# Kernel tuning notes

Hardware: AMD Instinct MI355X
Metric: run time of the kernel (lower is better)

## Reference

```python
import jax, jax.numpy as jnp
import numpy as np

H, N, CH, L = 256, 256, 1, 1024


def setup_inputs() -> dict:
    key = jax.random.key(0)
    k1, k2, k3, k4 = jax.random.split(key, 4)
    # Hurwitz-like A so the discretized dA is stable (|eig| < 1) over L powers
    A = 0.05 * jax.random.normal(k1, (H, N, N), jnp.float32) - jnp.eye(N, dtype=jnp.float32)
    B = jax.random.normal(k2, (H, N), jnp.float32)
    C = jax.random.normal(k3, (CH, H, N), jnp.float32)
    log_dt = jax.random.uniform(k4, (H,), jnp.float32,
                                minval=np.log(1e-3), maxval=np.log(1e-1))
    return {"A": A, "B": B, "C": C, "log_dt": log_dt}


def reference(A, B, C, log_dt):
    # Bilinear (Tustin) discretization:
    #   dA = (I - dt/2 A)^{-1} (I + dt/2 A),  dB = dt * (I - dt/2 A)^{-1} B
    dt = jnp.exp(log_dt)                                   # (H,)
    I = jnp.eye(A.shape[-1], dtype=A.dtype)
    A_bwd = I - (dt[:, None, None] / 2) * A                # (H, N, N)
    A_fwd = I + (dt[:, None, None] / 2) * A                # (H, N, N)
    dB = dt[:, None] * jnp.linalg.solve(A_bwd, B[..., None])[..., 0]   # (H, N)
    dA = jnp.linalg.solve(A_bwd, A_fwd)                    # (H, N, N)

    # Krylov kernel: k[c,h,l] = C[c,h,:] @ dA^l @ dB[h,:]
    def step(x, _):
        y = jnp.einsum('chn,hn->ch', C, x)                 # contract with C
        x_next = jnp.einsum('hmn,hn->hm', dA, x)           # advance state
        return x_next, y

    _, ys = jax.lax.scan(step, dB, None, length=L)         # ys: (L, CH, H)
    k = jnp.transpose(ys, (1, 2, 0))                       # (CH, H, L)
    return k
```

## Files before the change

kernel.cpp:

```cpp
#include <hip/hip_runtime.h>
#include <cstdint>
#include <cstddef>

#define NH 256
#define ND 256
#define NL 1024
#define NUV 16
#define NWV 64

typedef __attribute__((ext_vector_type(4))) float f32x4;
typedef __attribute__((ext_vector_type(8))) short short8;
typedef __attribute__((ext_vector_type(8))) unsigned short u16x8;
typedef __attribute__((ext_vector_type(4))) unsigned short u16x4;
typedef __attribute__((ext_vector_type(4))) unsigned int u32x4;

__device__ __forceinline__ float bfrec(unsigned short hi, unsigned short lo) {
  return __uint_as_float(((unsigned)hi) << 16) + __uint_as_float(((unsigned)lo) << 16);
}
__device__ __forceinline__ unsigned rne16(unsigned u) {
  return u + 0x7FFFu + ((u >> 16) & 1u);
}
__device__ __forceinline__ void bfsplit(float x, unsigned short& hi, unsigned short& lo) {
  unsigned u = __float_as_uint(x);
  unsigned r1 = rne16(u);
  hi = (unsigned short)(r1 >> 16);
  float lf = x - __uint_as_float(r1 & 0xFFFF0000u);
  unsigned r2 = rne16(__float_as_uint(lf));
  lo = (unsigned short)(r2 >> 16);
}
__device__ __forceinline__ void gload16(const void* g, void* l) {
  __builtin_amdgcn_global_load_lds(
      (const __attribute__((address_space(1))) unsigned int*)g,
      (__attribute__((address_space(3))) unsigned int*)l, 16, 0, 0);
}
__device__ __forceinline__ int ksw(int row) { return (row >> 1) & 3; }

__global__ __launch_bounds__(256) void prep_kernel(
    const float* __restrict__ A, const float* __restrict__ log_dt,
    unsigned short* __restrict__ Mhi, unsigned short* __restrict__ Mlo)
{
  size_t e0 = ((size_t)blockIdx.x * 256 + threadIdx.x) * 16;
  int h = (int)(e0 >> 16);
  float hdt = 0.5f * __expf(log_dt[h]);
  unsigned short hb[16], lb[16];
#pragma unroll
  for (int i = 0; i < 4; ++i) {
    f32x4 v = *(const f32x4*)(A + e0 + i * 4);
#pragma unroll
    for (int j = 0; j < 4; ++j) bfsplit(v[j] * hdt, hb[i * 4 + j], lb[i * 4 + j]);
  }
  unsigned ph[8], pl[8];
#pragma unroll
  for (int i = 0; i < 8; ++i) {
    ph[i] = (unsigned)hb[2 * i] | ((unsigned)hb[2 * i + 1] << 16);
    pl[i] = (unsigned)lb[2 * i] | ((unsigned)lb[2 * i + 1] << 16);
  }
  u32x4 a0 = {ph[0], ph[1], ph[2], ph[3]}, a1 = {ph[4], ph[5], ph[6], ph[7]};
  u32x4 b0 = {pl[0], pl[1], pl[2], pl[3]}, b1 = {pl[4], pl[5], pl[6], pl[7]};
  *(u32x4*)(Mhi + e0) = a0; *(u32x4*)(Mhi + e0 + 8) = a1;
  *(u32x4*)(Mlo + e0) = b0; *(u32x4*)(Mlo + e0 + 8) = b1;
}

template <int ADDX, int QOUT>
__global__ __launch_bounds__(256) void gemm128_kernel(
    const unsigned short* __restrict__ Xhi, const unsigned short* __restrict__ Xlo,
    const unsigned short* __restrict__ Yhi, const unsigned short* __restrict__ Ylo,
    unsigned short* __restrict__ Dhi, unsigned short* __restrict__ Dlo,
    unsigned short* __restrict__ Qhi, unsigned short* __restrict__ Qlo)
{
  __shared__ unsigned short lds[33792];
  int tid = threadIdx.x;
  int lane = tid & 63, w = tid >> 6;
  int bid = blockIdx.x;
  int h = bid & 255, part = bid >> 8;
  int m0 = (part >> 1) * 128, n0 = (part & 1) * 128;
  size_t mb = (size_t)h * 65536;

  f32x4 acc[2][8];
#pragma unroll
  for (int m = 0; m < 2; ++m)
#pragma unroll
    for (int n = 0; n < 8; ++n) { f32x4 z = {0.f, 0.f, 0.f, 0.f}; acc[m][n] = z; }

  auto STAGE = [&](int s, int kb) {
#pragma unroll
    for (int j = 0; j < 2; ++j) {
      int c = j * 256 + tid;
      {
        int row = c >> 2, sp = c & 3;
        size_t go = mb + (size_t)(m0 + row) * 256 + kb * 32 + ((sp ^ ksw(row)) << 3);
        gload16(Xhi + go, &lds[s * 8192 + c * 8]);
        gload16(Xlo + go, &lds[s * 8192 + 4096 + c * 8]);
      }
      {
        int k = c >> 4, ns = c & 15;
        size_t go = mb + (size_t)(kb * 32 + k) * 256 + n0 + ns * 8;
        gload16(Yhi + go, &lds[16384 + s * 8192 + c * 8]);
        gload16(Ylo + go, &lds[16384 + s * 8192 + 4096 + c * 8]);
      }
    }
  };

  STAGE(0, 0);
  __builtin_amdgcn_sched_barrier(0);

  int nn = tid & 127, kh = tid >> 7;
  int cur = 0;
  for (int kb = 0; kb < 8; ++kb) {
    int nxt = cur ^ 1;
    if (kb < 7) {
      STAGE(nxt, kb + 1);
      __builtin_amdgcn_sched_barrier(0);
      asm volatile("s_waitcnt vmcnt(8)" ::: "memory");
    } else {
      asm volatile("s_waitcnt vmcnt(0)" ::: "memory");
    }
    __builtin_amdgcn_sched_barrier(0);
    __builtin_amdgcn_s_barrier();
    __builtin_amdgcn_sched_barrier(0);

    unsigned short* yb = &lds[16384 + cur * 8192];
    unsigned short rh[16], rl[16];
#pragma unroll
    for (int i = 0; i < 16; ++i) {
      rh[i] = yb[(kh * 16 + i) * 128 + nn];
      rl[i] = yb[4096 + (kh * 16 + i) * 128 + nn];
    }
    asm volatile("s_waitcnt lgkmcnt(0)" ::: "memory");
    __builtin_amdgcn_sched_barrier(0);
    __builtin_amdgcn_s_barrier();
    __builtin_amdgcn_sched_barrier(0);

#pragma unroll
    for (int s2 = 0; s2 < 2; ++s2) {
      int sl = kh * 2 + s2;
      int off = nn * 32 + ((sl ^ ksw(nn)) << 3);
      u16x8 vh, vl;
#pragma unroll
      for (int e = 0; e < 8; ++e) { vh[e] = rh[s2 * 8 + e]; vl[e] = rl[s2 * 8 + e]; }
      *(u16x8*)&yb[off] = vh;
      *(u16x8*)&yb[4096 + off] = vl;
    }
    asm volatile("s_waitcnt lgkmcnt(0)" ::: "memory");
    __builtin_amdgcn_sched_barrier(0);
    __builtin_amdgcn_s_barrier();
    __builtin_amdgcn_sched_barrier(0);

    int kg = lane >> 4, li = lane & 15;
    const unsigned short* xb = &lds[cur * 8192];
    short8 bhi[8], blo[8];
#pragma unroll
    for (int n = 0; n < 8; ++n) {
      int rowN = n * 16 + li;
      int off = rowN * 32 + ((kg ^ ksw(rowN)) << 3);
      bhi[n] = *(const short8*)&yb[off];
      blo[n] = *(const short8*)&yb[4096 + off];
    }
    __builtin_amdgcn_s_setprio(1);
#pragma unroll
    for (int m = 0; m < 2; ++m) {
      int rowM = w * 32 + m * 16 + li;
      int off = rowM * 32 + ((kg ^ ksw(rowM)) << 3);
      short8 ahi = *(const short8*)&xb[off];
      short8 alo = *(const short8*)&xb[4096 + off];
#pragma unroll
      for (int n = 0; n < 8; ++n) {
        acc[m][n] = __builtin_amdgcn_mfma_f32_16x16x32_bf16(ahi, bhi[n], acc[m][n], 0, 0, 0);
        acc[m][n] = __builtin_amdgcn_mfma_f32_16x16x32_bf16(ahi, blo[n], acc[m][n], 0, 0, 0);
        acc[m][n] = __builtin_amdgcn_mfma_f32_16x16x32_bf16(alo, bhi[n], acc[m][n], 0, 0, 0);
      }
    }
    __builtin_amdgcn_s_setprio(0);
    __builtin_amdgcn_sched_barrier(0);
    __builtin_amdgcn_s_barrier();
    __builtin_amdgcn_sched_barrier(0);
    cur = nxt;
  }

  float* fb = (float*)lds;
  {
    int q0 = (lane >> 4) * 4, li = lane & 15;
#pragma unroll
    for (int m = 0; m < 2; ++m)
#pragma unroll
      for (int n = 0; n < 8; ++n)
#pragma unroll
        for (int q = 0; q < 4; ++q)
          fb[(w * 32 + m * 16 + q0 + q) * 132 + n * 16 + li] = acc[m][n][q];
  }
  __syncthreads();
  {
    int row = tid >> 1, half = tid & 1;
#pragma unroll 1
    for (int hp = 0; hp < 2; ++hp) {
      int c0 = half * 64 + hp * 32;
      float v[32];
#pragma unroll
      for (int u = 0; u < 8; ++u) {
        f32x4 t4 = *(const f32x4*)&fb[row * 132 + c0 + u * 4];
#pragma unroll
        for (int e = 0; e < 4; ++e) v[u * 4 + e] = t4[e];
      }
      size_t go = mb + (size_t)(m0 + row) * 256 + n0 + c0;
      float xv[32];
      if (ADDX || QOUT) {
#pragma unroll
        for (int u = 0; u < 4; ++u) {
          u16x8 xh = *(const u16x8*)(Xhi + go + u * 8);
          u16x8 xl = *(const u16x8*)(Xlo + go + u * 8);
#pragma unroll
          for (int e = 0; e < 8; ++e) xv[u * 8 + e] = bfrec(xh[e], xl[e]);
        }
        if (ADDX) {
#pragma unroll
          for (int e = 0; e < 32; ++e) v[e] += xv[e];
        }
      }
      {
        unsigned hw[16], lw[16];
#pragma unroll
        for (int i = 0; i < 16; ++i) {
          unsigned short ha, la, hb2, lb2;
          bfsplit(v[2 * i], ha, la);
          bfsplit(v[2 * i + 1], hb2, lb2);
          hw[i] = (unsigned)ha | ((unsigned)hb2 << 16);
          lw[i] = (unsigned)la | ((unsigned)lb2 << 16);
        }
#pragma unroll
        for (int u = 0; u < 4; ++u) {
          u32x4 a = {hw[u * 4], hw[u * 4 + 1], hw[u * 4 + 2], hw[u * 4 + 3]};
          u32x4 b = {lw[u * 4], lw[u * 4 + 1], lw[u * 4 + 2], lw[u * 4 + 3]};
          *(u32x4*)(Dhi + go + u * 8) = a;
          *(u32x4*)(Dlo + go + u * 8) = b;
        }
      }
      if (QOUT) {
        int grow = m0 + row, gc0 = n0 + c0;
        float qv[32];
#pragma unroll
        for (int e = 0; e < 32; ++e)
          qv[e] = v[e] + 2.f * xv[e] + ((gc0 + e) == grow ? 1.f : 0.f);
        unsigned hw[16], lw[16];
#pragma unroll
        for (int i = 0; i < 16; ++i) {
          unsigned short ha, la, hb2, lb2;
          bfsplit(qv[2 * i], ha, la);
          bfsplit(qv[2 * i + 1], hb2, lb2);
          hw[i] = (unsigned)ha | ((unsigned)hb2 << 16);
          lw[i] = (unsigned)la | ((unsigned)lb2 << 16);
        }
#pragma unroll
        for (int u = 0; u < 4; ++u) {
          u32x4 a = {hw[u * 4], hw[u * 4 + 1], hw[u * 4 + 2], hw[u * 4 + 3]};
          u32x4 b = {lw[u * 4], lw[u * 4 + 1], lw[u * 4 + 2], lw[u * 4 + 3]};
          *(u32x4*)(Qhi + go + u * 8) = a;
          *(u32x4*)(Qlo + go + u * 8) = b;
        }
      }
    }
  }
}

__global__ __launch_bounds__(256) void db_kernel(
    const unsigned short* __restrict__ dAhi, const unsigned short* __restrict__ dAlo,
    const float* __restrict__ Bv, const float* __restrict__ log_dt, float* __restrict__ dB)
{
  int h = blockIdx.x, r = threadIdx.x;
  __shared__ float bl[256];
  bl[r] = Bv[h * 256 + r];
  __syncthreads();
  const unsigned short* ph = dAhi + (size_t)h * 65536 + (size_t)r * 256;
  const unsigned short* pl = dAlo + (size_t)h * 65536 + (size_t)r * 256;
  float acc = bl[r];
  for (int c8 = 0; c8 < 32; ++c8) {
    u16x8 vh = *(const u16x8*)(ph + c8 * 8);
    u16x8 vl = *(const u16x8*)(pl + c8 * 8);
#pragma unroll
    for (int e = 0; e < 8; ++e) acc += bfrec(vh[e], vl[e]) * bl[c8 * 8 + e];
  }
  dB[h * 256 + r] = 0.5f * __expf(log_dt[h]) * acc;
}

__device__ __forceinline__ int physc(int c) { return c + ((c >> 4) << 2); }

__global__ __launch_bounds__(1024) void chain_kernel(
    const unsigned short* __restrict__ dAhi, const unsigned short* __restrict__ dAlo,
    const unsigned short* __restrict__ Ghi, const unsigned short* __restrict__ Glo,
    const float* __restrict__ Cin, const float* __restrict__ dB,
    float* __restrict__ U, float* __restrict__ W)
{
  int b = blockIdx.x;
  bool um = b < NH;
  int h = um ? b : b - NH;
  const float* x0 = um ? (Cin + (size_t)h * 256) : (dB + (size_t)h * 256);
  float* out = um ? (U + (size_t)h * (NUV * 256)) : (W + (size_t)h * (NWV * 256));
  int nv = um ? NUV : NWV;

  int tid = threadIdx.x;
  int rg = tid >> 4, cg = tid & 15;
  float mat[4][16];
  if (um) {
    const unsigned short* mh = dAhi + (size_t)h * 65536;
    const unsigned short* ml = dAlo + (size_t)h * 65536;
#pragma unroll
    for (int j = 0; j < 16; ++j) {
      u16x4 h4 = *(const u16x4*)(mh + (size_t)(cg * 16 + j) * 256 + rg * 4);
      u16x4 l4 = *(const u16x4*)(ml + (size_t)(cg * 16 + j) * 256 + rg * 4);
#pragma unroll
      for (int rr = 0; rr < 4; ++rr) mat[rr][j] = bfrec(h4[rr], l4[rr]);
    }
  } else {
    const unsigned short* mh = Ghi + (size_t)h * 65536;
    const unsigned short* ml = Glo + (size_t)h * 65536;
#pragma unroll
    for (int rr = 0; rr < 4; ++rr) {
      const unsigned short* ph = mh + (size_t)(rg * 4 + rr) * 256 + cg * 16;
      const unsigned short* pl = ml + (size_t)(rg * 4 + rr) * 256 + cg * 16;
      u16x8 h0 = *(const u16x8*)ph, h1 = *(const u16x8*)(ph + 8);
      u16x8 l0 = *(const u16x8*)pl, l1 = *(const u16x8*)(pl + 8);
#pragma unroll
      for (int e = 0; e < 8; ++e) {
        mat[rr][e] = bfrec(h0[e], l0[e]);
        mat[rr][8 + e] = bfrec(h1[e], l1[e]);
      }
    }
  }
  __shared__ float xb[2][320];
  if (tid < 256) {
    float vv = x0[tid];
    xb[0][physc(tid)] = vv;
    out[tid] = vv;
  }
  __syncthreads();
  int p = 0;
  for (int v = 1; v < nv; ++v) {
    float part[4] = {0.f, 0.f, 0.f, 0.f};
#pragma unroll
    for (int sl = 0; sl < 4; ++sl) {
      f32x4 xv = *(const f32x4*)&xb[p][cg * 20 + sl * 4];
#pragma unroll
      for (int rr = 0; rr < 4; ++rr)
#pragma unroll
        for (int e = 0; e < 4; ++e) part[rr] += mat[rr][sl * 4 + e] * xv[e];
    }
#pragma unroll
    for (int rr = 0; rr < 4; ++rr) {
      part[rr] += __shfl_xor(part[rr], 1, 64);
      part[rr] += __shfl_xor(part[rr], 2, 64);
      part[rr] += __shfl_xor(part[rr], 4, 64);
      part[rr] += __shfl_xor(part[rr], 8, 64);
    }
    float val = (cg == 0) ? part[0] : ((cg == 1) ? part[1] : ((cg == 2) ? part[2] : part[3]));
    if (cg < 4) {
      int row = rg * 4 + cg;
      xb[p ^ 1][physc(row)] = val;
      out[(size_t)v * 256 + row] = val;
    }
    __syncthreads();
    p ^= 1;
  }
}

__global__ __launch_bounds__(512) void gram_kernel(
    const float* __restrict__ U, const float* __restrict__ W, float* __restrict__ out)
{
  int b = blockIdx.x;
  int h = b >> 1, jh = b & 1;
  __shared__ float ul[16][260];
  __shared__ float wl[32][260];
  int tid = threadIdx.x;
  const float* Up = U + (size_t)h * (NUV * 256);
  const float* Wp = W + (size_t)h * (NWV * 256) + (size_t)jh * 32 * 256;
  {
    int r = tid >> 5, cb = (tid & 31) * 8;
    f32x4 a = *(const f32x4*)(Up + (size_t)r * 256 + cb);
    f32x4 c2 = *(const f32x4*)(Up + (size_t)r * 256 + cb + 4);
    *(f32x4*)&ul[r][cb] = a;
    *(f32x4*)&ul[r][cb + 4] = c2;
  }
  {
    int r = tid >> 4, cb = (tid & 15) * 16;
#pragma unroll
    for (int u = 0; u < 4; ++u) {
      f32x4 a = *(const f32x4*)(Wp + (size_t)r * 256 + cb + u * 4);
      *(f32x4*)&wl[r][cb + u * 4] = a;
    }
  }
  __syncthreads();
  int i = tid >> 5, j2 = tid & 31;
  float acc = 0.f;
#pragma unroll 8
  for (int c = 0; c < 256; c += 4) {
    f32x4 uu = *(const f32x4*)&ul[i][c];
    f32x4 ww = *(const f32x4*)&wl[j2][c];
    acc += uu[0] * ww[0] + uu[1] * ww[1] + uu[2] * ww[2] + uu[3] * ww[3];
  }
  out[(size_t)h * 1024 + (size_t)(jh * 32 + j2) * 16 + i] = acc;
}

__global__ void bail_kernel(float* out, unsigned mib) {
  if (threadIdx.x == 0) out[blockIdx.x] = -(2.0e6f + (float)mib * 4096.0f);
}

extern "C" void kernel_launch(void* const* d_in, const int* in_sizes, int n_in,
                              void* d_out, int out_size, void* d_ws, size_t ws_size,
                              hipStream_t stream) {
  const float* A = (const float*)d_in[0];
  const float* B = (const float*)d_in[1];
  const float* C = (const float*)d_in[2];
  const float* log_dt = (const float*)d_in[3];
  float* out = (float*)d_out;

  const size_t BUF = (size_t)NH * ND * ND * 2 * 2;
  const size_t HALF = (size_t)NH * ND * ND;
  const size_t VEC = (size_t)NH * ND * 4;
  const size_t USZ = (size_t)NH * NUV * ND * 4;
  const size_t WSZ = (size_t)NH * NWV * ND * 4;
  const size_t NEED3 = 3 * BUF + VEC + USZ + WSZ;
  if (ws_size < NEED3) {
    bail_kernel<<<8, 64, 0, stream>>>(out, (unsigned)(ws_size >> 20));
    return;
  }
  uint8_t* w8 = (uint8_t*)d_ws;
  auto HI = [&](int b) -> unsigned short* { return (unsigned short*)(w8 + (size_t)b * BUF); };
  auto LO = [&](int b) -> unsigned short* { return HI(b) + HALF; };
  float* dBp = (float*)(w8 + 3 * BUF);
  float* Up = (float*)(w8 + 3 * BUF + VEC);
  float* Wp = (float*)(w8 + 3 * BUF + VEC + USZ);

  prep_kernel<<<4096, 256, 0, stream>>>(A, log_dt, HI(0), LO(0));
  gemm128_kernel<0, 1><<<1024, 256, 0, stream>>>(HI(0), LO(0), HI(0), LO(0),
                                                 HI(1), LO(1), HI(2), LO(2));
  gemm128_kernel<1, 0><<<1024, 256, 0, stream>>>(HI(2), LO(2), HI(1), LO(1),
                                                 HI(0), LO(0), nullptr, nullptr);
  gemm128_kernel<0, 0><<<1024, 256, 0, stream>>>(HI(1), LO(1), HI(1), LO(1),
                                                 HI(2), LO(2), nullptr, nullptr);
  gemm128_kernel<1, 0><<<1024, 256, 0, stream>>>(HI(0), LO(0), HI(2), LO(2),
                                                 HI(1), LO(1), nullptr, nullptr);
  db_kernel<<<NH, 256, 0, stream>>>(HI(1), LO(1), B, log_dt, dBp);
  gemm128_kernel<0, 0><<<1024, 256, 0, stream>>>(HI(1), LO(1), HI(1), LO(1),
                                                 HI(0), LO(0), nullptr, nullptr);
  gemm128_kernel<0, 0><<<1024, 256, 0, stream>>>(HI(0), LO(0), HI(0), LO(0),
                                                 HI(2), LO(2), nullptr, nullptr);
  gemm128_kernel<0, 0><<<1024, 256, 0, stream>>>(HI(2), LO(2), HI(2), LO(2),
                                                 HI(0), LO(0), nullptr, nullptr);
  gemm128_kernel<0, 0><<<1024, 256, 0, stream>>>(HI(0), LO(0), HI(0), LO(0),
                                                 HI(2), LO(2), nullptr, nullptr);
  chain_kernel<<<2 * NH, 1024, 0, stream>>>(HI(1), LO(1), HI(2), LO(2), C, dBp, Up, Wp);
  gram_kernel<<<2 * NH, 512, 0, stream>>>(Up, Wp, out);
}
```

Before: 650.3 us.

## Emit transposed GEMM outputs so consumers load B operand K-contiguous, skipping LDS transpose

The GEMM kernel gains template flags to also write a transposed copy of its result. Later GEMMs can then read the Y operand already in K-contiguous layout and drop the in-LDS transpose step with its extra barriers. The chain kernel is split so the U/W power chains read pre-transposed or row-major matrices directly. Workspace tiers pick how many planes are available, falling back to the old schedule when memory is short. The extra transposed stores add write traffic and memory footprint in exchange for cheaper GEMM inner loops.

```diff
diff --git a/kernel.cpp b/kernel.cpp
--- a/kernel.cpp
+++ b/kernel.cpp
@@ -61,11 +61,12 @@
   *(u32x4*)(Mlo + e0) = b0; *(u32x4*)(Mlo + e0 + 8) = b1;
 }
 
-template <int ADDX, int QOUT>
+template <int YT, int ADDX, int OUTN, int OUTT, int QOUT>
 __global__ __launch_bounds__(256) void gemm128_kernel(
     const unsigned short* __restrict__ Xhi, const unsigned short* __restrict__ Xlo,
     const unsigned short* __restrict__ Yhi, const unsigned short* __restrict__ Ylo,
     unsigned short* __restrict__ Dhi, unsigned short* __restrict__ Dlo,
+    unsigned short* __restrict__ DThi, unsigned short* __restrict__ DTlo,
     unsigned short* __restrict__ Qhi, unsigned short* __restrict__ Qlo)
 {
   __shared__ unsigned short lds[33792];
@@ -86,17 +87,28 @@
 #pragma unroll
     for (int j = 0; j < 2; ++j) {
       int c = j * 256 + tid;
-      {
+      if (YT) {
         int row = c >> 2, sp = c & 3;
-        size_t go = mb + (size_t)(m0 + row) * 256 + kb * 32 + ((sp ^ ksw(row)) << 3);
-        gload16(Xhi + go, &lds[s * 8192 + c * 8]);
-        gload16(Xlo + go, &lds[s * 8192 + 4096 + c * 8]);
-      }
-      {
-        int k = c >> 4, ns = c & 15;
-        size_t go = mb + (size_t)(kb * 32 + k) * 256 + n0 + ns * 8;
-        gload16(Yhi + go, &lds[16384 + s * 8192 + c * 8]);
-        gload16(Ylo + go, &lds[16384 + s * 8192 + 4096 + c * 8]);
+        int koff = kb * 32 + ((sp ^ ksw(row)) << 3);
+        size_t gx = mb + (size_t)(m0 + row) * 256 + koff;
+        size_t gy = mb + (size_t)(n0 + row) * 256 + koff;
+        gload16(Xhi + gx, &lds[s * 8192 + c * 8]);
+        gload16(Xlo + gx, &lds[s * 8192 + 4096 + c * 8]);
+        gload16(Yhi + gy, &lds[16384 + s * 8192 + c * 8]);
+        gload16(Ylo + gy, &lds[16384 + s * 8192 + 4096 + c * 8]);
+      } else {
+        {
+          int row = c >> 2, sp = c & 3;
+          size_t go = mb + (size_t)(m0 + row) * 256 + kb * 32 + ((sp ^ ksw(row)) << 3);
+          gload16(Xhi + go, &lds[s * 8192 + c * 8]);
+          gload16(Xlo + go, &lds[s * 8192 + 4096 + c * 8]);
+        }
+        {
+          int k = c >> 4, ns = c & 15;
+          size_t go = mb + (size_t)(kb * 32 + k) * 256 + n0 + ns * 8;
+          gload16(Yhi + go, &lds[16384 + s * 8192 + c * 8]);
+          gload16(Ylo + go, &lds[16384 + s * 8192 + 4096 + c * 8]);
+        }
       }
     }
   };
@@ -120,31 +132,32 @@
     __builtin_amdgcn_sched_barrier(0);
 
     unsigned short* yb = &lds[16384 + cur * 8192];
-    unsigned short rh[16], rl[16];
-#pragma unroll
-    for (int i = 0; i < 16; ++i) {
-      rh[i] = yb[(kh * 16 + i) * 128 + nn];
-      rl[i] = yb[4096 + (kh * 16 + i) * 128 + nn];
-    }
-    asm volatile("s_waitcnt lgkmcnt(0)" ::: "memory");
-    __builtin_amdgcn_sched_barrier(0);
-    __builtin_amdgcn_s_barrier();
-    __builtin_amdgcn_sched_barrier(0);
-
-#pragma unroll
-    for (int s2 = 0; s2 < 2; ++s2) {
-      int sl = kh * 2 + s2;
-      int off = nn * 32 + ((sl ^ ksw(nn)) << 3);
-      u16x8 vh, vl;
-#pragma unroll
-      for (int e = 0; e < 8; ++e) { vh[e] = rh[s2 * 8 + e]; vl[e] = rl[s2 * 8 + e]; }
-      *(u16x8*)&yb[off] = vh;
-      *(u16x8*)&yb[4096 + off] = vl;
-    }
-    asm volatile("s_waitcnt lgkmcnt(0)" ::: "memory");
-    __builtin_amdgcn_sched_barrier(0);
-    __builtin_amdgcn_s_barrier();
-    __builtin_amdgcn_sched_barrier(0);
+    if (!YT) {
+      unsigned short rh[16], rl[16];
+#pragma unroll
+      for (int i = 0; i < 16; ++i) {
+        rh[i] = yb[(kh * 16 + i) * 128 + nn];
+        rl[i] = yb[4096 + (kh * 16 + i) * 128 + nn];
+      }
+      asm volatile("s_waitcnt lgkmcnt(0)" ::: "memory");
+      __builtin_amdgcn_sched_barrier(0);
+      __builtin_amdgcn_s_barrier();
+      __builtin_amdgcn_sched_barrier(0);
+#pragma unroll
+      for (int s2 = 0; s2 < 2; ++s2) {
+        int sl = kh * 2 + s2;
+        int off = nn * 32 + ((sl ^ ksw(nn)) << 3);
+        u16x8 vh, vl;
+#pragma unroll
+        for (int e = 0; e < 8; ++e) { vh[e] = rh[s2 * 8 + e]; vl[e] = rl[s2 * 8 + e]; }
+        *(u16x8*)&yb[off] = vh;
+        *(u16x8*)&yb[4096 + off] = vl;
+      }
+      asm volatile("s_waitcnt lgkmcnt(0)" ::: "memory");
+      __builtin_amdgcn_sched_barrier(0);
+      __builtin_amdgcn_s_barrier();
+      __builtin_amdgcn_sched_barrier(0);
+    }
 
     int kg = lane >> 4, li = lane & 15;
     const unsigned short* xb = &lds[cur * 8192];
@@ -189,7 +202,7 @@
           fb[(w * 32 + m * 16 + q0 + q) * 132 + n * 16 + li] = acc[m][n][q];
   }
   __syncthreads();
-  {
+  if (OUTN || ADDX) {
     int row = tid >> 1, half = tid & 1;
 #pragma unroll 1
     for (int hp = 0; hp < 2; ++hp) {
@@ -214,9 +227,18 @@
         if (ADDX) {
 #pragma unroll
           for (int e = 0; e < 32; ++e) v[e] += xv[e];
-        }
-      }
-      {
+          if (OUTT) {
+#pragma unroll
+            for (int u = 0; u < 8; ++u) {
+              f32x4 t4;
+#pragma unroll
+              for (int e = 0; e < 4; ++e) t4[e] = v[u * 4 + e];
+              *(f32x4*)&fb[row * 132 + c0 + u * 4] = t4;
+            }
+          }
+        }
+      }
+      if (OUTN) {
         unsigned hw[16], lw[16];
 #pragma unroll
         for (int i = 0; i < 16; ++i) {
@@ -256,6 +278,34 @@
           *(u32x4*)(Qhi + go + u * 8) = a;
           *(u32x4*)(Qlo + go + u * 8) = b;
         }
+      }
+    }
+  }
+  if (OUTT) {
+    if (ADDX) __syncthreads();
+    int c = tid & 127, rh2 = tid >> 7;
+#pragma unroll 1
+    for (int ch2 = 0; ch2 < 2; ++ch2) {
+      int r0 = rh2 * 64 + ch2 * 32;
+      float tv[32];
+#pragma unroll
+      for (int i = 0; i < 32; ++i) tv[i] = fb[(r0 + i) * 132 + c];
+      unsigned hw[16], lw[16];
+#pragma unroll
+      for (int i = 0; i < 16; ++i) {
+        unsigned short ha, la, hb2, lb2;
+        bfsplit(tv[2 * i], ha, la);
+        bfsplit(tv[2 * i + 1], hb2, lb2);
+        hw[i] = (unsigned)ha | ((unsigned)hb2 << 16);
+        lw[i] = (unsigned)la | ((unsigned)lb2 << 16);
+      }
+      size_t go = mb + (size_t)(n0 + c) * 256 + m0 + r0;
+#pragma unroll
+      for (int u = 0; u < 4; ++u) {
+        u32x4 a = {hw[u * 4], hw[u * 4 + 1], hw[u * 4 + 2], hw[u * 4 + 3]};
+        u32x4 b = {lw[u * 4], lw[u * 4 + 1], lw[u * 4 + 2], lw[u * 4 + 3]};
+        *(u32x4*)(DThi + go + u * 8) = a;
+        *(u32x4*)(DTlo + go + u * 8) = b;
       }
     }
   }
@@ -283,7 +333,73 @@
 
 __device__ __forceinline__ int physc(int c) { return c + ((c >> 4) << 2); }
 
-__global__ __launch_bounds__(1024) void chain_kernel(
+__global__ __launch_bounds__(1024) void chainAB_kernel(
+    const unsigned short* __restrict__ UTh, const unsigned short* __restrict__ UTl,
+    const unsigned short* __restrict__ Gh, const unsigned short* __restrict__ Gl,
+    const float* __restrict__ Cin, const float* __restrict__ dB,
+    float* __restrict__ U, float* __restrict__ W, int base)
+{
+  int b = blockIdx.x + base;
+  bool um = b < NH;
+  int h = um ? b : b - NH;
+  const unsigned short* mh = (um ? UTh : Gh) + (size_t)h * 65536;
+  const unsigned short* ml = (um ? UTl : Gl) + (size_t)h * 65536;
+  const float* x0 = um ? (Cin + (size_t)h * 256) : (dB + (size_t)h * 256);
+  float* out = um ? (U + (size_t)h * (NUV * 256)) : (W + (size_t)h * (NWV * 256));
+  int nv = um ? NUV : NWV;
+
+  int tid = threadIdx.x;
+  int rg = tid >> 4, cg = tid & 15;
+  float mat[4][16];
+#pragma unroll
+  for (int rr = 0; rr < 4; ++rr) {
+    const unsigned short* ph = mh + (size_t)(rg * 4 + rr) * 256 + cg * 16;
+    const unsigned short* pl = ml + (size_t)(rg * 4 + rr) * 256 + cg * 16;
+    u16x8 h0 = *(const u16x8*)ph, h1 = *(const u16x8*)(ph + 8);
+    u16x8 l0 = *(const u16x8*)pl, l1 = *(const u16x8*)(pl + 8);
+#pragma unroll
+    for (int e = 0; e < 8; ++e) {
+      mat[rr][e] = bfrec(h0[e], l0[e]);
+      mat[rr][8 + e] = bfrec(h1[e], l1[e]);
+    }
+  }
+  __shared__ float xb[2][320];
+  if (tid < 256) {
+    float vv = x0[tid];
+    xb[0][physc(tid)] = vv;
+    out[tid] = vv;
+  }
+  __syncthreads();
+  int p = 0;
+  for (int v = 1; v < nv; ++v) {
+    float part[4] = {0.f, 0.f, 0.f, 0.f};
+#pragma unroll
+    for (int sl = 0; sl < 4; ++sl) {
+      f32x4 xv = *(const f32x4*)&xb[p][cg * 20 + sl * 4];
+#pragma unroll
+      for (int rr = 0; rr < 4; ++rr)
+#pragma unroll
+        for (int e = 0; e < 4; ++e) part[rr] += mat[rr][sl * 4 + e] * xv[e];
+    }
+#pragma unroll
+    for (int rr = 0; rr < 4; ++rr) {
+      part[rr] += __shfl_xor(part[rr], 1, 64);
+      part[rr] += __shfl_xor(part[rr], 2, 64);
+      part[rr] += __shfl_xor(part[rr], 4, 64);
+      part[rr] += __shfl_xor(part[rr], 8, 64);
+    }
+    float val = (cg == 0) ? part[0] : ((cg == 1) ? part[1] : ((cg == 2) ? part[2] : part[3]));
+    if (cg < 4) {
+      int row = rg * 4 + cg;
+      xb[p ^ 1][physc(row)] = val;
+      out[(size_t)v * 256 + row] = val;
+    }
+    __syncthreads();
+    p ^= 1;
+  }
+}
+
+__global__ __launch_bounds__(1024) void chainC_kernel(
     const unsigned short* __restrict__ dAhi, const unsigned short* __restrict__ dAlo,
     const unsigned short* __restrict__ Ghi, const unsigned short* __restrict__ Glo,
     const float* __restrict__ Cin, const float* __restrict__ dB,
@@ -411,41 +527,95 @@
   const float* log_dt = (const float*)d_in[3];
   float* out = (float*)d_out;
 
-  const size_t BUF = (size_t)NH * ND * ND * 2 * 2;
-  const size_t HALF = (size_t)NH * ND * ND;
+  const size_t PLANE = (size_t)NH * ND * ND * 2;
+  const size_t PHALF = (size_t)NH * ND * ND;
   const size_t VEC = (size_t)NH * ND * 4;
   const size_t USZ = (size_t)NH * NUV * ND * 4;
   const size_t WSZ = (size_t)NH * NWV * ND * 4;
-  const size_t NEED3 = 3 * BUF + VEC + USZ + WSZ;
-  if (ws_size < NEED3) {
+  const size_t EXTRA = VEC + USZ + WSZ;
+  const size_t NEED_A = 10 * PLANE + EXTRA;
+  const size_t NEED_B = 8 * PLANE + EXTRA;
+  const size_t NEED_C = 6 * PLANE + EXTRA;
+  if (ws_size < NEED_C) {
     bail_kernel<<<8, 64, 0, stream>>>(out, (unsigned)(ws_size >> 20));
     return;
   }
   uint8_t* w8 = (uint8_t*)d_ws;
-  auto HI = [&](int b) -> unsigned short* { return (unsigned short*)(w8 + (size_t)b * BUF); };
-  auto LO = [&](int b) -> unsigned short* { return HI(b) + HALF; };
-  float* dBp = (float*)(w8 + 3 * BUF);
-  float* Up = (float*)(w8 + 3 * BUF + VEC);
-  float* Wp = (float*)(w8 + 3 * BUF + VEC + USZ);
-
-  prep_kernel<<<4096, 256, 0, stream>>>(A, log_dt, HI(0), LO(0));
-  gemm128_kernel<0, 1><<<1024, 256, 0, stream>>>(HI(0), LO(0), HI(0), LO(0),
-                                                 HI(1), LO(1), HI(2), LO(2));
-  gemm128_kernel<1, 0><<<1024, 256, 0, stream>>>(HI(2), LO(2), HI(1), LO(1),
-                                                 HI(0), LO(0), nullptr, nullptr);
-  gemm128_kernel<0, 0><<<1024, 256, 0, stream>>>(HI(1), LO(1), HI(1), LO(1),
-                                                 HI(2), LO(2), nullptr, nullptr);
-  gemm128_kernel<1, 0><<<1024, 256, 0, stream>>>(HI(0), LO(0), HI(2), LO(2),
-                                                 HI(1), LO(1), nullptr, nullptr);
-  db_kernel<<<NH, 256, 0, stream>>>(HI(1), LO(1), B, log_dt, dBp);
-  gemm128_kernel<0, 0><<<1024, 256, 0, stream>>>(HI(1), LO(1), HI(1), LO(1),
-                                                 HI(0), LO(0), nullptr, nullptr);
-  gemm128_kernel<0, 0><<<1024, 256, 0, stream>>>(HI(0), LO(0), HI(0), LO(0),
-                                                 HI(2), LO(2), nullptr, nullptr);
-  gemm128_kernel<0, 0><<<1024, 256, 0, stream>>>(HI(2), LO(2), HI(2), LO(2),
-                                                 HI(0), LO(0), nullptr, nullptr);
-  gemm128_kernel<0, 0><<<1024, 256, 0, stream>>>(HI(0), LO(0), HI(0), LO(0),
-                                                 HI(2), LO(2), nullptr, nullptr);
-  chain_kernel<<<2 * NH, 1024, 0, stream>>>(HI(1), LO(1), HI(2), LO(2), C, dBp, Up, Wp);
-  gram_kernel<<<2 * NH, 512, 0, stream>>>(Up, Wp, out);
-}
+  auto P = [&](int i) -> unsigned short* { return (unsigned short*)(w8 + (size_t)i * PLANE); };
+
+  if (ws_size >= NEED_B) {
+    bool tierA = (ws_size >= NEED_A);
+    int np = tierA ? 10 : 8;
+    float* dBp = (float*)(w8 + (size_t)np * PLANE);
+    float* Up = (float*)(w8 + (size_t)np * PLANE + VEC);
+    float* Wp = (float*)(w8 + (size_t)np * PLANE + VEC + USZ);
+    prep_kernel<<<4096, 256, 0, stream>>>(A, log_dt, P(0), P(1));
+    if (tierA) {
+      gemm128_kernel<0, 0, 1, 1, 1><<<1024, 256, 0, stream>>>(
+          P(0), P(1), P(0), P(1), P(2), P(3), P(4), P(5), P(6), P(7));
+      gemm128_kernel<1, 1, 1, 0, 0><<<1024, 256, 0, stream>>>(
+          P(6), P(7), P(4), P(5), P(8), P(9), nullptr, nullptr, nullptr, nullptr);
+      gemm128_kernel<1, 0, 0, 1, 0><<<1024, 256, 0, stream>>>(
+          P(2), P(3), P(4), P(5), nullptr, nullptr, P(0), P(1), nullptr, nullptr);
+      gemm128_kernel<1, 1, 1, 1, 0><<<1024, 256, 0, stream>>>(
+          P(8), P(9), P(0), P(1), P(2), P(3), P(4), P(5), nullptr, nullptr);
+      db_kernel<<<NH, 256, 0, stream>>>(P(2), P(3), B, log_dt, dBp);
+      gemm128_kernel<1, 0, 1, 1, 0><<<1024, 256, 0, stream>>>(
+          P(2), P(3), P(4), P(5), P(6), P(7), P(8), P(9), nullptr, nullptr);
+      gemm128_kernel<1, 0, 1, 1, 0><<<1024, 256, 0, stream>>>(
+          P(6), P(7), P(8), P(9), P(0), P(1), P(2), P(3), nullptr, nullptr);
+      gemm128_kernel<1, 0, 1, 1, 0><<<1024, 256, 0, stream>>>(
+          P(0), P(1), P(2), P(3), P(6), P(7), P(8), P(9), nullptr, nullptr);
+      gemm128_kernel<1, 0, 1, 0, 0><<<1024, 256, 0, stream>>>(
+          P(6), P(7), P(8), P(9), P(0), P(1), nullptr, nullptr, nullptr, nullptr);
+      chainAB_kernel<<<2 * NH, 1024, 0, stream>>>(P(4), P(5), P(0), P(1), C, dBp, Up, Wp, 0);
+    } else {
+      gemm128_kernel<0, 0, 1, 1, 1><<<1024, 256, 0, stream>>>(
+          P(0), P(1), P(0), P(1), P(2), P(3), P(4), P(5), P(6), P(7));
+      gemm128_kernel<1, 1, 1, 0, 0><<<1024, 256, 0, stream>>>(
+          P(6), P(7), P(4), P(5), P(0), P(1), nullptr, nullptr, nullptr, nullptr);
+      gemm128_kernel<1, 0, 0, 1, 0><<<1024, 256, 0, stream>>>(
+          P(2), P(3), P(4), P(5), nullptr, nullptr, P(6), P(7), nullptr, nullptr);
+      gemm128_kernel<1, 1, 1, 1, 0><<<1024, 256, 0, stream>>>(
+          P(0), P(1), P(6), P(7), P(2), P(3), P(4), P(5), nullptr, nullptr);
+      db_kernel<<<NH, 256, 0, stream>>>(P(2), P(3), B, log_dt, dBp);
+      chainAB_kernel<<<NH, 1024, 0, stream>>>(P(4), P(5), P(4), P(5), C, dBp, Up, Wp, 0);
+      gemm128_kernel<1, 0, 1, 1, 0><<<1024, 256, 0, stream>>>(
+          P(2), P(3), P(4), P(5), P(0), P(1), P(6), P(7), nullptr, nullptr);
+      gemm128_kernel<1, 0, 1, 1, 0><<<1024, 256, 0, stream>>>(
+          P(0), P(1), P(6), P(7), P(2), P(3), P(4), P(5), nullptr, nullptr);
+      gemm128_kernel<1, 0, 1, 1, 0><<<1024, 256, 0, stream>>>(
+          P(2), P(3), P(4), P(5), P(0), P(1), P(6), P(7), nullptr, nullptr);
+      gemm128_kernel<1, 0, 1, 0, 0><<<1024, 256, 0, stream>>>(
+          P(0), P(1), P(6), P(7), P(2), P(3), nullptr, nullptr, nullptr, nullptr);
+      chainAB_kernel<<<NH, 1024, 0, stream>>>(P(2), P(3), P(2), P(3), C, dBp, Up, Wp, NH);
+    }
+    gram_kernel<<<2 * NH, 512, 0, stream>>>(Up, Wp, out);
+  } else {
+    float* dBp = (float*)(w8 + 6 * PLANE);
+    float* Up = (float*)(w8 + 6 * PLANE + VEC);
+    float* Wp = (float*)(w8 + 6 * PLANE + VEC + USZ);
+    auto HI = [&](int b2) -> unsigned short* { return P(2 * b2); };
+    auto LO = [&](int b2) -> unsigned short* { return P(2 * b2) + PHALF; };
+    prep_kernel<<<4096, 256, 0, stream>>>(A, log_dt, HI(0), LO(0));
+    gemm128_kernel<0, 0, 1, 0, 1><<<1024, 256, 0, stream>>>(
+        HI(0), LO(0), HI(0), LO(0), HI(1), LO(1), nullptr, nullptr, HI(2), LO(2));
+    gemm128_kernel<0, 1, 1, 0, 0><<<1024, 256, 0, stream>>>(
+        HI(2), LO(2), HI(1), LO(1), HI(0), LO(0), nullptr, nullptr, nullptr, nullptr);
+    gemm128_kernel<0, 0, 1, 0, 0><<<1024, 256, 0, stream>>>(
+        HI(1), LO(1), HI(1), LO(1), HI(2), LO(2), nullptr, nullptr, nullptr, nullptr);
+    gemm128_kernel<0, 1, 1, 0, 0><<<1024, 256, 0, stream>>>(
+        HI(0), LO(0), HI(2), LO(2), HI(1), LO(1), nullptr, nullptr, nullptr, nullptr);
+    db_kernel<<<NH, 256, 0, stream>>>(HI(1), LO(1), B, log_dt, dBp);
+    gemm128_kernel<0, 0, 1, 0, 0><<<1024, 256, 0, stream>>>(
+        HI(1), LO(1), HI(1), LO(1), HI(0), LO(0), nullptr, nullptr, nullptr, nullptr);
+    gemm128_kernel<0, 0, 1, 0, 0><<<1024, 256, 0, stream>>>(
+        HI(0), LO(0), HI(0), LO(0), HI(2), LO(2), nullptr, nullptr, nullptr, nullptr);
+    gemm128_kernel<0, 0, 1, 0, 0><<<1024, 256, 0, stream>>>(
+        HI(2), LO(2), HI(2), LO(2), HI(0), LO(0), nullptr, nullptr, nullptr, nullptr);
+    gemm128_kernel<0, 0, 1, 0, 0><<<1024, 256, 0, stream>>>(
+        HI(0), LO(0), HI(0), LO(0), HI(2), LO(2), nullptr, nullptr, nullptr, nullptr);
+    chainC_kernel<<<2 * NH, 1024, 0, stream>>>(HI(1), LO(1), HI(2), LO(2), C, dBp, Up, Wp);
+    gram_kernel<<<2 * NH, 512, 0, stream>>>(Up, Wp, out);
+  }
+}
```

New measurement: 650.9 us. About the same (+0.1%).

## Rebalance Krylov split to 32x32 vectors, fold identity add into GEMM B-operand

Applied to the files above, without the earlier changes.

Changes the Krylov decomposition so both the C-side and dB-side chains produce 32 vectors each instead of 16 and 64. This needs one extra squaring GEMM (dA^32 instead of dA^16) but shortens the longest sequential matrix-vector chain. The X+XY epilogue is replaced by adding the identity into the Y operand during LDS staging, X(I+Y), which removes the extra global read of X in the epilogue. Block-to-head mapping is also reordered so blocks that share a head run closer together, which should help cache reuse. The workspace is reorganised into six planes.

```diff
diff --git a/kernel.cpp b/kernel.cpp
--- a/kernel.cpp
+++ b/kernel.cpp
@@ -4,9 +4,7 @@
 
 #define NH 256
 #define ND 256
-#define NL 1024
-#define NUV 16
-#define NWV 64
+#define NSV 32
 
 typedef __attribute__((ext_vector_type(4))) float f32x4;
 typedef __attribute__((ext_vector_type(8))) short short8;
@@ -61,7 +59,7 @@
   *(u32x4*)(Mlo + e0) = b0; *(u32x4*)(Mlo + e0 + 8) = b1;
 }
 
-template <int ADDX, int QOUT>
+template <int YI, int QOUT>
 __global__ __launch_bounds__(256) void gemm128_kernel(
     const unsigned short* __restrict__ Xhi, const unsigned short* __restrict__ Xlo,
     const unsigned short* __restrict__ Yhi, const unsigned short* __restrict__ Ylo,
@@ -72,7 +70,8 @@
   int tid = threadIdx.x;
   int lane = tid & 63, w = tid >> 6;
   int bid = blockIdx.x;
-  int h = bid & 255, part = bid >> 8;
+  int part = (bid >> 3) & 3;
+  int h = ((bid >> 5) << 3) | (bid & 7);
   int m0 = (part >> 1) * 128, n0 = (part & 1) * 128;
   size_t mb = (size_t)h * 65536;
 
@@ -137,7 +136,16 @@
       int off = nn * 32 + ((sl ^ ksw(nn)) << 3);
       u16x8 vh, vl;
 #pragma unroll
-      for (int e = 0; e < 8; ++e) { vh[e] = rh[s2 * 8 + e]; vl[e] = rl[s2 * 8 + e]; }
+      for (int e = 0; e < 8; ++e) {
+        unsigned short hh = rh[s2 * 8 + e], ll = rl[s2 * 8 + e];
+        if (YI) {
+          if (kb * 32 + kh * 16 + s2 * 8 + e == n0 + nn) {
+            float vv = bfrec(hh, ll) + 1.0f;
+            bfsplit(vv, hh, ll);
+          }
+        }
+        vh[e] = hh; vl[e] = ll;
+      }
       *(u16x8*)&yb[off] = vh;
       *(u16x8*)&yb[4096 + off] = vl;
     }
@@ -202,20 +210,6 @@
         for (int e = 0; e < 4; ++e) v[u * 4 + e] = t4[e];
       }
       size_t go = mb + (size_t)(m0 + row) * 256 + n0 + c0;
-      float xv[32];
-      if (ADDX || QOUT) {
-#pragma unroll
-        for (int u = 0; u < 4; ++u) {
-          u16x8 xh = *(const u16x8*)(Xhi + go + u * 8);
-          u16x8 xl = *(const u16x8*)(Xlo + go + u * 8);
-#pragma unroll
-          for (int e = 0; e < 8; ++e) xv[u * 8 + e] = bfrec(xh[e], xl[e]);
-        }
-        if (ADDX) {
-#pragma unroll
-          for (int e = 0; e < 32; ++e) v[e] += xv[e];
-        }
-      }
       {
         unsigned hw[16], lw[16];
 #pragma unroll
@@ -235,6 +229,14 @@
         }
       }
       if (QOUT) {
+        float xv[32];
+#pragma unroll
+        for (int u = 0; u < 4; ++u) {
+          u16x8 xh = *(const u16x8*)(Xhi + go + u * 8);
+          u16x8 xl = *(const u16x8*)(Xlo + go + u * 8);
+#pragma unroll
+          for (int e = 0; e < 8; ++e) xv[u * 8 + e] = bfrec(xh[e], xl[e]);
+        }
         int grow = m0 + row, gc0 = n0 + c0;
         float qv[32];
 #pragma unroll
@@ -283,7 +285,7 @@
 
 __device__ __forceinline__ int physc(int c) { return c + ((c >> 4) << 2); }
 
-__global__ __launch_bounds__(1024) void chain_kernel(
+__global__ __launch_bounds__(1024) void chain32_kernel(
     const unsigned short* __restrict__ dAhi, const unsigned short* __restrict__ dAlo,
     const unsigned short* __restrict__ Ghi, const unsigned short* __restrict__ Glo,
     const float* __restrict__ Cin, const float* __restrict__ dB,
@@ -293,8 +295,7 @@
   bool um = b < NH;
   int h = um ? b : b - NH;
   const float* x0 = um ? (Cin + (size_t)h * 256) : (dB + (size_t)h * 256);
-  float* out = um ? (U + (size_t)h * (NUV * 256)) : (W + (size_t)h * (NWV * 256));
-  int nv = um ? NUV : NWV;
+  float* out = (um ? U : W) + (size_t)h * (NSV * 256);
 
   int tid = threadIdx.x;
   int rg = tid >> 4, cg = tid & 15;
@@ -333,7 +334,7 @@
   }
   __syncthreads();
   int p = 0;
-  for (int v = 1; v < nv; ++v) {
+  for (int v = 1; v < NSV; ++v) {
     float part[4] = {0.f, 0.f, 0.f, 0.f};
 #pragma unroll
     for (int sl = 0; sl < 4; ++sl) {
@@ -366,28 +367,28 @@
 {
   int b = blockIdx.x;
   int h = b >> 1, jh = b & 1;
-  __shared__ float ul[16][260];
-  __shared__ float wl[32][260];
+  __shared__ float ul[32][260];
+  __shared__ float wl[16][260];
   int tid = threadIdx.x;
-  const float* Up = U + (size_t)h * (NUV * 256);
-  const float* Wp = W + (size_t)h * (NWV * 256) + (size_t)jh * 32 * 256;
+  const float* Up = U + (size_t)h * (NSV * 256);
+  const float* Wp = W + (size_t)h * (NSV * 256) + (size_t)jh * 16 * 256;
+  {
+    int r = tid >> 4, cb = (tid & 15) * 16;
+#pragma unroll
+    for (int u = 0; u < 4; ++u) {
+      f32x4 a = *(const f32x4*)(Up + (size_t)r * 256 + cb + u * 4);
+      *(f32x4*)&ul[r][cb + u * 4] = a;
+    }
+  }
   {
     int r = tid >> 5, cb = (tid & 31) * 8;
-    f32x4 a = *(const f32x4*)(Up + (size_t)r * 256 + cb);
-    f32x4 c2 = *(const f32x4*)(Up + (size_t)r * 256 + cb + 4);
-    *(f32x4*)&ul[r][cb] = a;
-    *(f32x4*)&ul[r][cb + 4] = c2;
-  }
-  {
-    int r = tid >> 4, cb = (tid & 15) * 16;
-#pragma unroll
-    for (int u = 0; u < 4; ++u) {
-      f32x4 a = *(const f32x4*)(Wp + (size_t)r * 256 + cb + u * 4);
-      *(f32x4*)&wl[r][cb + u * 4] = a;
-    }
+    f32x4 a = *(const f32x4*)(Wp + (size_t)r * 256 + cb);
+    f32x4 c2 = *(const f32x4*)(Wp + (size_t)r * 256 + cb + 4);
+    *(f32x4*)&wl[r][cb] = a;
+    *(f32x4*)&wl[r][cb + 4] = c2;
   }
   __syncthreads();
-  int i = tid >> 5, j2 = tid & 31;
+  int i = tid & 31, j2 = tid >> 5;
   float acc = 0.f;
 #pragma unroll 8
   for (int c = 0; c < 256; c += 4) {
@@ -395,7 +396,7 @@
     f32x4 ww = *(const f32x4*)&wl[j2][c];
     acc += uu[0] * ww[0] + uu[1] * ww[1] + uu[2] * ww[2] + uu[3] * ww[3];
   }
-  out[(size_t)h * 1024 + (size_t)(jh * 32 + j2) * 16 + i] = acc;
+  out[(size_t)h * 1024 + (size_t)(jh * 16 + j2) * 32 + i] = acc;
 }
 
 __global__ void bail_kernel(float* out, unsigned mib) {
@@ -411,41 +412,41 @@
   const float* log_dt = (const float*)d_in[3];
   float* out = (float*)d_out;
 
-  const size_t BUF = (size_t)NH * ND * ND * 2 * 2;
-  const size_t HALF = (size_t)NH * ND * ND;
+  const size_t PLANE = (size_t)NH * ND * ND * 2;
   const size_t VEC = (size_t)NH * ND * 4;
-  const size_t USZ = (size_t)NH * NUV * ND * 4;
-  const size_t WSZ = (size_t)NH * NWV * ND * 4;
-  const size_t NEED3 = 3 * BUF + VEC + USZ + WSZ;
-  if (ws_size < NEED3) {
+  const size_t USZ = (size_t)NH * NSV * ND * 4;
+  const size_t WSZ = USZ;
+  const size_t NEED = 6 * PLANE + VEC + USZ + WSZ;
+  if (ws_size < NEED) {
     bail_kernel<<<8, 64, 0, stream>>>(out, (unsigned)(ws_size >> 20));
     return;
   }
   uint8_t* w8 = (uint8_t*)d_ws;
-  auto HI = [&](int b) -> unsigned short* { return (unsigned short*)(w8 + (size_t)b * BUF); };
-  auto LO = [&](int b) -> unsigned short* { return HI(b) + HALF; };
-  float* dBp = (float*)(w8 + 3 * BUF);
-  float* Up = (float*)(w8 + 3 * BUF + VEC);
-  float* Wp = (float*)(w8 + 3 * BUF + VEC + USZ);
-
-  prep_kernel<<<4096, 256, 0, stream>>>(A, log_dt, HI(0), LO(0));
-  gemm128_kernel<0, 1><<<1024, 256, 0, stream>>>(HI(0), LO(0), HI(0), LO(0),
-                                                 HI(1), LO(1), HI(2), LO(2));
-  gemm128_kernel<1, 0><<<1024, 256, 0, stream>>>(HI(2), LO(2), HI(1), LO(1),
-                                                 HI(0), LO(0), nullptr, nullptr);
-  gemm128_kernel<0, 0><<<1024, 256, 0, stream>>>(HI(1), LO(1), HI(1), LO(1),
-                                                 HI(2), LO(2), nullptr, nullptr);
-  gemm128_kernel<1, 0><<<1024, 256, 0, stream>>>(HI(0), LO(0), HI(2), LO(2),
-                                                 HI(1), LO(1), nullptr, nullptr);
-  db_kernel<<<NH, 256, 0, stream>>>(HI(1), LO(1), B, log_dt, dBp);
-  gemm128_kernel<0, 0><<<1024, 256, 0, stream>>>(HI(1), LO(1), HI(1), LO(1),
-                                                 HI(0), LO(0), nullptr, nullptr);
-  gemm128_kernel<0, 0><<<1024, 256, 0, stream>>>(HI(0), LO(0), HI(0), LO(0),
-                                                 HI(2), LO(2), nullptr, nullptr);
-  gemm128_kernel<0, 0><<<1024, 256, 0, stream>>>(HI(2), LO(2), HI(2), LO(2),
-                                                 HI(0), LO(0), nullptr, nullptr);
-  gemm128_kernel<0, 0><<<1024, 256, 0, stream>>>(HI(0), LO(0), HI(0), LO(0),
-                                                 HI(2), LO(2), nullptr, nullptr);
-  chain_kernel<<<2 * NH, 1024, 0, stream>>>(HI(1), LO(1), HI(2), LO(2), C, dBp, Up, Wp);
+  auto P = [&](int i) -> unsigned short* { return (unsigned short*)(w8 + (size_t)i * PLANE); };
+  float* dBp = (float*)(w8 + 6 * PLANE);
+  float* Up = (float*)(w8 + 6 * PLANE + VEC);
+  float* Wp = (float*)(w8 + 6 * PLANE + VEC + USZ);
+
+  prep_kernel<<<4096, 256, 0, stream>>>(A, log_dt, P(0), P(1));
+  gemm128_kernel<0, 1><<<1024, 256, 0, stream>>>(P(0), P(1), P(0), P(1),
+                                                 P(2), P(3), P(4), P(5));
+  gemm128_kernel<1, 0><<<1024, 256, 0, stream>>>(P(4), P(5), P(2), P(3),
+                                                 P(0), P(1), nullptr, nullptr);
+  gemm128_kernel<0, 0><<<1024, 256, 0, stream>>>(P(2), P(3), P(2), P(3),
+                                                 P(4), P(5), nullptr, nullptr);
+  gemm128_kernel<1, 0><<<1024, 256, 0, stream>>>(P(0), P(1), P(4), P(5),
+                                                 P(2), P(3), nullptr, nullptr);
+  db_kernel<<<NH, 256, 0, stream>>>(P(2), P(3), B, log_dt, dBp);
+  gemm128_kernel<0, 0><<<1024, 256, 0, stream>>>(P(2), P(3), P(2), P(3),
+                                                 P(0), P(1), nullptr, nullptr);
+  gemm128_kernel<0, 0><<<1024, 256, 0, stream>>>(P(0), P(1), P(0), P(1),
+                                                 P(4), P(5), nullptr, nullptr);
+  gemm128_kernel<0, 0><<<1024, 256, 0, stream>>>(P(4), P(5), P(4), P(5),
+                                                 P(0), P(1), nullptr, nullptr);
+  gemm128_kernel<0, 0><<<1024, 256, 0, stream>>>(P(0), P(1), P(0), P(1),
+                                                 P(4), P(5), nullptr, nullptr);
+  gemm128_kernel<0, 0><<<1024, 256, 0, stream>>>(P(4), P(5), P(4), P(5),
+                                                 P(0), P(1), nullptr, nullptr);
+  chain32_kernel<<<2 * NH, 1024, 0, stream>>>(P(2), P(3), P(0), P(1), C, dBp, Up, Wp);
   gram_kernel<<<2 * NH, 512, 0, stream>>>(Up, Wp, out);
 }
```

After: 624.0 us. 1.04x faster.
